# Performance work log

Measured on AMD Instinct MI355X. Metric: run time of the kernel, lower is better.

## Reference

```python
import jax, jax.numpy as jnp
import numpy as np

INPUT_LAYER_SIZE = 40960 * 2
LAYER1_SIZE = 512
LAYER2_SIZE = 32
LAYER3_SIZE = 32
BATCH = 4096


def setup_inputs() -> dict:
    key = jax.random.key(0)
    ks = jax.random.split(key, 10)
    # Sparse one-hot style features: mostly zeros with ~30 active entries per side.
    def sparse_features(k, n_active=30):
        kidx, = jax.random.split(k, 1)
        idx = jax.random.randint(kidx, (BATCH, n_active), 0, 40960)
        feats = jnp.zeros((BATCH, 40960), dtype=jnp.float32)
        return feats.at[jnp.arange(BATCH)[:, None], idx].set(1.0)
    w_features = sparse_features(ks[0])
    b_features = sparse_features(ks[1])
    s_in = 1.0 / np.sqrt(INPUT_LAYER_SIZE)
    s1 = 1.0 / np.sqrt(LAYER1_SIZE)
    s2 = 1.0 / np.sqrt(LAYER2_SIZE)
    s3 = 1.0 / np.sqrt(LAYER3_SIZE)
    return {
        "w_features": w_features,
        "b_features": b_features,
        "W_in": jax.random.uniform(ks[2], (LAYER1_SIZE, INPUT_LAYER_SIZE), jnp.float32, -s_in, s_in),
        "b_in": jax.random.uniform(ks[3], (LAYER1_SIZE,), jnp.float32, -s_in, s_in),
        "W1": jax.random.uniform(ks[4], (LAYER2_SIZE, LAYER1_SIZE), jnp.float32, -s1, s1),
        "b1": jax.random.uniform(ks[5], (LAYER2_SIZE,), jnp.float32, -s1, s1),
        "W2": jax.random.uniform(ks[6], (LAYER3_SIZE, LAYER2_SIZE), jnp.float32, -s2, s2),
        "b2": jax.random.uniform(ks[7], (LAYER3_SIZE,), jnp.float32, -s2, s2),
        "W3": jax.random.uniform(ks[8], (1, LAYER3_SIZE), jnp.float32, -s3, s3),
        "b3": jax.random.uniform(ks[9], (1,), jnp.float32, -s3, s3),
    }


def reference(w_features, b_features, W_in, b_in, W1, b1, W2, b2, W3, b3):
    # Concatenate both perspectives: [B, 81920]
    x = jnp.concatenate([w_features, b_features], axis=1)
    # Huge sparse-input accumulator layer (the kernel-headroom op)
    accum = x @ W_in.T + b_in                       # [B, 512]
    l1 = jnp.clip(accum, 0.0, 1.0)                  # clipped ReLU
    l2 = jnp.clip(l1 @ W1.T + b1, 0.0, 1.0)         # [B, 32]
    l3 = jnp.clip(l2 @ W2.T + b2, 0.0, 1.0)         # [B, 32]
    return l3 @ W3.T + b3                           # [B, 1]
```

## Files before the change

kernel.cpp:

```cpp
#include <hip/hip_runtime.h>
#include <hip/hip_bf16.h>

#define IN_PER_SIDE   40960
#define IN_TOTAL      81920
#define L1            512
#define L2            32
#define L3_           32
#define BATCH         4096
#define MAXIDX        128

typedef float    v4f __attribute__((ext_vector_type(4)));
typedef float    v8f __attribute__((ext_vector_type(8)));
typedef _Float16 v4h __attribute__((ext_vector_type(4)));
typedef _Float16 v8h __attribute__((ext_vector_type(8)));

#define WT_BYTES ((size_t)IN_TOTAL * L1 * sizeof(_Float16))

__global__ __launch_bounds__(256) void transpose_win(
    const float* __restrict__ W, _Float16* __restrict__ WTh)
{
    __shared__ float tile[64][65];
    const int jt = blockIdx.x * 64;
    const int ot = blockIdx.y * 64;
    const int tx = threadIdx.x & 15;
    const int ty = threadIdx.x >> 4;

#pragma unroll
    for (int k = 0; k < 4; ++k) {
        const int o = ty + 16 * k;
        const v4f* p = (const v4f*)&W[(size_t)(ot + o) * IN_TOTAL + jt + 4 * tx];
        v4f v = __builtin_nontemporal_load(p);
        tile[4 * tx + 0][o] = v.x;
        tile[4 * tx + 1][o] = v.y;
        tile[4 * tx + 2][o] = v.z;
        tile[4 * tx + 3][o] = v.w;
    }
    __syncthreads();
#pragma unroll
    for (int k = 0; k < 4; ++k) {
        const int j = ty + 16 * k;
        v4f v;
        v.x = tile[j][4 * tx + 0];
        v.y = tile[j][4 * tx + 1];
        v.z = tile[j][4 * tx + 2];
        v.w = tile[j][4 * tx + 3];
        v4h h = __builtin_convertvector(v, v4h);
        *(v4h*)&WTh[(size_t)(jt + j) * L1 + ot + 4 * tx] = h;
    }
}

__global__ __launch_bounds__(512) void nnue_fused(
    const float* __restrict__ wf, const float* __restrict__ bfeat,
    const _Float16* __restrict__ WTh,
    const float* __restrict__ b_in,
    const float* __restrict__ W1, const float* __restrict__ b1,
    const float* __restrict__ W2, const float* __restrict__ b2,
    const float* __restrict__ W3, const float* __restrict__ b3,
    float* __restrict__ out)
{
    const int b = blockIdx.x;
    const int t = threadIdx.x;

    __shared__ int   sidx[MAXIDX];
    __shared__ int   scnt;
    __shared__ float accs[8 * 64 * 9];
    __shared__ float l1s[L1];
    __shared__ float l2acc[L2];
    __shared__ float l2s[L2];
    __shared__ float l3s[L3_];

    if (t == 0) scnt = 0;
    __syncthreads();

    const v4f* wrow = (const v4f*)(wf    + (size_t)b * IN_PER_SIDE);
    const v4f* brow = (const v4f*)(bfeat + (size_t)b * IN_PER_SIDE);
    const int nvec = IN_PER_SIDE / 4;

    for (int i = t; i < nvec; i += 512) {
        v4f v = __builtin_nontemporal_load(wrow + i);
        if (v.x + v.y + v.z + v.w != 0.0f) {
            if (v.x != 0.0f) sidx[atomicAdd(&scnt, 1)] = 4 * i + 0;
            if (v.y != 0.0f) sidx[atomicAdd(&scnt, 1)] = 4 * i + 1;
            if (v.z != 0.0f) sidx[atomicAdd(&scnt, 1)] = 4 * i + 2;
            if (v.w != 0.0f) sidx[atomicAdd(&scnt, 1)] = 4 * i + 3;
        }
        v4f u = __builtin_nontemporal_load(brow + i);
        if (u.x + u.y + u.z + u.w != 0.0f) {
            if (u.x != 0.0f) sidx[atomicAdd(&scnt, 1)] = IN_PER_SIDE + 4 * i + 0;
            if (u.y != 0.0f) sidx[atomicAdd(&scnt, 1)] = IN_PER_SIDE + 4 * i + 1;
            if (u.z != 0.0f) sidx[atomicAdd(&scnt, 1)] = IN_PER_SIDE + 4 * i + 2;
            if (u.w != 0.0f) sidx[atomicAdd(&scnt, 1)] = IN_PER_SIDE + 4 * i + 3;
        }
    }
    __syncthreads();

    const int n = scnt;
    const int w = t >> 6;
    const int l = t & 63;
    const v8h* WTH8 = (const v8h*)WTh;

    v8f acc0 = {0,0,0,0,0,0,0,0};
    v8f acc1 = {0,0,0,0,0,0,0,0};
    int k = w;
    for (; k + 16 <= n; k += 16) {
        v8h h0 = WTH8[(size_t)sidx[k]     * 64 + l];
        v8h h1 = WTH8[(size_t)sidx[k + 8] * 64 + l];
        acc0 += __builtin_convertvector(h0, v8f);
        acc1 += __builtin_convertvector(h1, v8f);
    }
    for (; k < n; k += 8)
        acc0 += __builtin_convertvector(WTH8[(size_t)sidx[k] * 64 + l], v8f);
    acc0 += acc1;

    {
        float* dst = &accs[(w * 64 + l) * 9];
#pragma unroll
        for (int i = 0; i < 8; ++i) dst[i] = acc0[i];
    }
    __syncthreads();

    {
        const int ll = t >> 3, c = t & 7;
        float s = 0.0f;
#pragma unroll
        for (int ww = 0; ww < 8; ++ww) s += accs[(ww * 64 + ll) * 9 + c];
        l1s[t] = fminf(fmaxf(s + b_in[t], 0.0f), 1.0f);
    }
    __syncthreads();

    {
        const int kk = t >> 4;
        const int gg = t & 15;
        const float* wp = W1 + (size_t)kk * L1;
        float p = 0.0f;
        for (int o = gg; o < L1; o += 16) p += wp[o] * l1s[o];
#pragma unroll
        for (int off = 8; off > 0; off >>= 1) p += __shfl_down(p, off, 16);
        if (gg == 0) l2acc[kk] = p;
    }
    __syncthreads();
    if (t < L2) l2s[t] = fminf(fmaxf(l2acc[t] + b1[t], 0.0f), 1.0f);
    __syncthreads();

    if (t < L3_) {
        const float* wp = W2 + (size_t)t * L2;
        float p = b2[t];
#pragma unroll
        for (int q = 0; q < L2; ++q) p += wp[q] * l2s[q];
        l3s[t] = fminf(fmaxf(p, 0.0f), 1.0f);
    }
    __syncthreads();

    if (t == 0) {
        float p = b3[0];
#pragma unroll
        for (int q = 0; q < L3_; ++q) p += W3[q] * l3s[q];
        out[b] = p;
    }
}

__global__ __launch_bounds__(512) void nnue_fallback(
    const float* __restrict__ wf, const float* __restrict__ bfeat,
    const float* __restrict__ W_in, const float* __restrict__ b_in,
    const float* __restrict__ W1, const float* __restrict__ b1,
    const float* __restrict__ W2, const float* __restrict__ b2,
    const float* __restrict__ W3, const float* __restrict__ b3,
    float* __restrict__ out)
{
    const int b = blockIdx.x;
    const int t = threadIdx.x;
    __shared__ int   idxs[MAXIDX];
    __shared__ int   scnt;
    __shared__ float l1s[L1];
    __shared__ float l2acc[L2];
    __shared__ float l2s[L2];
    __shared__ float l3s[L3_];

    if (t == 0) scnt = 0;
    __syncthreads();
    const v4f* wrow = (const v4f*)(wf    + (size_t)b * IN_PER_SIDE);
    const v4f* brow = (const v4f*)(bfeat + (size_t)b * IN_PER_SIDE);
    for (int i = t; i < IN_PER_SIDE / 4; i += 512) {
        v4f v = wrow[i];
        if (v.x != 0.0f) idxs[atomicAdd(&scnt, 1)] = 4 * i + 0;
        if (v.y != 0.0f) idxs[atomicAdd(&scnt, 1)] = 4 * i + 1;
        if (v.z != 0.0f) idxs[atomicAdd(&scnt, 1)] = 4 * i + 2;
        if (v.w != 0.0f) idxs[atomicAdd(&scnt, 1)] = 4 * i + 3;
        v4f u = brow[i];
        if (u.x != 0.0f) idxs[atomicAdd(&scnt, 1)] = IN_PER_SIDE + 4 * i + 0;
        if (u.y != 0.0f) idxs[atomicAdd(&scnt, 1)] = IN_PER_SIDE + 4 * i + 1;
        if (u.z != 0.0f) idxs[atomicAdd(&scnt, 1)] = IN_PER_SIDE + 4 * i + 2;
        if (u.w != 0.0f) idxs[atomicAdd(&scnt, 1)] = IN_PER_SIDE + 4 * i + 3;
    }
    __syncthreads();
    const int n = scnt;
    float a0 = 0.0f;
    const float* row = W_in + (size_t)t * IN_TOTAL;
    for (int i = 0; i < n; ++i) a0 += row[idxs[i]];
    l1s[t] = fminf(fmaxf(b_in[t] + a0, 0.0f), 1.0f);
    __syncthreads();
    {
        const int k = t >> 4, g = t & 15;
        const float* wp = W1 + (size_t)k * L1;
        float p = 0.0f;
        for (int o = g; o < L1; o += 16) p += wp[o] * l1s[o];
#pragma unroll
        for (int off = 8; off > 0; off >>= 1) p += __shfl_down(p, off, 16);
        if (g == 0) l2acc[k] = p;
    }
    __syncthreads();
    if (t < L2) l2s[t] = fminf(fmaxf(l2acc[t] + b1[t], 0.0f), 1.0f);
    __syncthreads();
    if (t < L3_) {
        const float* wp = W2 + (size_t)t * L2;
        float p = b2[t];
#pragma unroll
        for (int q = 0; q < L2; ++q) p += wp[q] * l2s[q];
        l3s[t] = fminf(fmaxf(p, 0.0f), 1.0f);
    }
    __syncthreads();
    if (t == 0) {
        float p = b3[0];
#pragma unroll
        for (int q = 0; q < L3_; ++q) p += W3[q] * l3s[q];
        out[b] = p;
    }
}

extern "C" void kernel_launch(void* const* d_in, const int* in_sizes, int n_in,
                              void* d_out, int out_size, void* d_ws, size_t ws_size,
                              hipStream_t stream) {
    const float* wf   = (const float*)d_in[0];
    const float* bfeat= (const float*)d_in[1];
    const float* W_in = (const float*)d_in[2];
    const float* b_in = (const float*)d_in[3];
    const float* W1   = (const float*)d_in[4];
    const float* b1   = (const float*)d_in[5];
    const float* W2   = (const float*)d_in[6];
    const float* b2   = (const float*)d_in[7];
    const float* W3   = (const float*)d_in[8];
    const float* b3   = (const float*)d_in[9];
    float* out = (float*)d_out;

    if (ws_size >= WT_BYTES) {
        _Float16* WTh = (_Float16*)d_ws;
        dim3 grid(IN_TOTAL / 64, L1 / 64);
        transpose_win<<<grid, 256, 0, stream>>>(W_in, WTh);
        nnue_fused<<<BATCH, 512, 0, stream>>>(
            wf, bfeat, WTh, b_in, W1, b1, W2, b2, W3, b3, out);
    } else {
        nnue_fallback<<<BATCH, 512, 0, stream>>>(
            wf, bfeat, W_in, b_in, W1, b1, W2, b2, W3, b3, out);
    }
}
```

Before: 1.303 ms.

## Fuse weight transpose into main kernel with work-stealing tiles and global barrier

Merges the separate W_in transpose/fp16 conversion kernel into the main NNUE kernel: blocks dynamically claim transpose tiles through a global atomic counter, then scan their feature rows, then spin-wait until all tiles are done before gathering. The goal is to overlap the feature-row scanning with the transpose and remove a kernel launch boundary. It adds a memset launch, a grid-wide spin barrier that relies on all claiming blocks being resident or finishing (deadlock risk if the grid is oversubscribed and late blocks wait while unfinished tiles have not been claimed), and shared-memory union reuse.

```diff
diff --git a/kernel.cpp b/kernel.cpp
--- a/kernel.cpp
+++ b/kernel.cpp
@@ -8,6 +8,7 @@
 #define L3_           32
 #define BATCH         4096
 #define MAXIDX        128
+#define NTILES        10240
 
 typedef float    v4f __attribute__((ext_vector_type(4)));
 typedef float    v8f __attribute__((ext_vector_type(8)));
@@ -15,43 +16,12 @@
 typedef _Float16 v8h __attribute__((ext_vector_type(8)));
 
 #define WT_BYTES ((size_t)IN_TOTAL * L1 * sizeof(_Float16))
-
-__global__ __launch_bounds__(256) void transpose_win(
-    const float* __restrict__ W, _Float16* __restrict__ WTh)
-{
-    __shared__ float tile[64][65];
-    const int jt = blockIdx.x * 64;
-    const int ot = blockIdx.y * 64;
-    const int tx = threadIdx.x & 15;
-    const int ty = threadIdx.x >> 4;
-
-#pragma unroll
-    for (int k = 0; k < 4; ++k) {
-        const int o = ty + 16 * k;
-        const v4f* p = (const v4f*)&W[(size_t)(ot + o) * IN_TOTAL + jt + 4 * tx];
-        v4f v = __builtin_nontemporal_load(p);
-        tile[4 * tx + 0][o] = v.x;
-        tile[4 * tx + 1][o] = v.y;
-        tile[4 * tx + 2][o] = v.z;
-        tile[4 * tx + 3][o] = v.w;
-    }
-    __syncthreads();
-#pragma unroll
-    for (int k = 0; k < 4; ++k) {
-        const int j = ty + 16 * k;
-        v4f v;
-        v.x = tile[j][4 * tx + 0];
-        v.y = tile[j][4 * tx + 1];
-        v.z = tile[j][4 * tx + 2];
-        v.w = tile[j][4 * tx + 3];
-        v4h h = __builtin_convertvector(v, v4h);
-        *(v4h*)&WTh[(size_t)(jt + j) * L1 + ot + 4 * tx] = h;
-    }
-}
-
-__global__ __launch_bounds__(512) void nnue_fused(
+#define CTR_BYTES 128
+
+__global__ __launch_bounds__(512) void nnue_all(
+    const float* __restrict__ W, _Float16* __restrict__ WTh,
+    int* __restrict__ ctrs,
     const float* __restrict__ wf, const float* __restrict__ bfeat,
-    const _Float16* __restrict__ WTh,
     const float* __restrict__ b_in,
     const float* __restrict__ W1, const float* __restrict__ b1,
     const float* __restrict__ W2, const float* __restrict__ b2,
@@ -61,16 +31,60 @@
     const int b = blockIdx.x;
     const int t = threadIdx.x;
 
+    __shared__ union {
+        float tile[64][65];
+        float accs[8 * 64 * 9];
+    } sh;
     __shared__ int   sidx[MAXIDX];
     __shared__ int   scnt;
-    __shared__ float accs[8 * 64 * 9];
+    __shared__ int   stile;
     __shared__ float l1s[L1];
     __shared__ float l2acc[L2];
     __shared__ float l2s[L2];
     __shared__ float l3s[L3_];
 
+    int* claim_ctr = ctrs;
+    int* done_ctr  = ctrs + 16;
+
     if (t == 0) scnt = 0;
-    __syncthreads();
+
+    int my = 0;
+    for (;;) {
+        if (t == 0) stile = atomicAdd(claim_ctr, 1);
+        __syncthreads();
+        const int tile_id = stile;
+        if (tile_id >= NTILES) break;
+        ++my;
+        const int jt = (tile_id % 1280) * 64;
+        const int ot = (tile_id / 1280) * 64;
+        {
+            const int tx = t & 15, o = t >> 4;
+#pragma unroll
+            for (int k = 0; k < 2; ++k) {
+                const int oo = o + 32 * k;
+                const v4f* p = (const v4f*)&W[(size_t)(ot + oo) * IN_TOTAL + jt + 4 * tx];
+                v4f v = __builtin_nontemporal_load(p);
+                sh.tile[4 * tx + 0][oo] = v.x;
+                sh.tile[4 * tx + 1][oo] = v.y;
+                sh.tile[4 * tx + 2][oo] = v.z;
+                sh.tile[4 * tx + 3][oo] = v.w;
+            }
+        }
+        __syncthreads();
+        {
+            const int j = t >> 3, c0 = (t & 7) * 8;
+            v8f vf;
+#pragma unroll
+            for (int i = 0; i < 8; ++i) vf[i] = sh.tile[j][c0 + i];
+            v8h h = __builtin_convertvector(vf, v8h);
+            *(v8h*)&WTh[(size_t)(jt + j) * L1 + ot + c0] = h;
+        }
+        __syncthreads();
+    }
+    if (my > 0 && t == 0) {
+        __threadfence();
+        atomicAdd(done_ctr, my);
+    }
 
     const v4f* wrow = (const v4f*)(wf    + (size_t)b * IN_PER_SIDE);
     const v4f* brow = (const v4f*)(bfeat + (size_t)b * IN_PER_SIDE);
@@ -91,6 +105,13 @@
             if (u.z != 0.0f) sidx[atomicAdd(&scnt, 1)] = IN_PER_SIDE + 4 * i + 2;
             if (u.w != 0.0f) sidx[atomicAdd(&scnt, 1)] = IN_PER_SIDE + 4 * i + 3;
         }
+    }
+
+    if (t == 0) {
+        while (__hip_atomic_load(done_ctr, __ATOMIC_RELAXED,
+                                 __HIP_MEMORY_SCOPE_AGENT) < NTILES)
+            __builtin_amdgcn_s_sleep(2);
+        __threadfence();
     }
     __syncthreads();
 
@@ -113,7 +134,7 @@
     acc0 += acc1;
 
     {
-        float* dst = &accs[(w * 64 + l) * 9];
+        float* dst = &sh.accs[(w * 64 + l) * 9];
 #pragma unroll
         for (int i = 0; i < 8; ++i) dst[i] = acc0[i];
     }
@@ -123,7 +144,7 @@
         const int ll = t >> 3, c = t & 7;
         float s = 0.0f;
 #pragma unroll
-        for (int ww = 0; ww < 8; ++ww) s += accs[(ww * 64 + ll) * 9 + c];
+        for (int ww = 0; ww < 8; ++ww) s += sh.accs[(ww * 64 + ll) * 9 + c];
         l1s[t] = fminf(fmaxf(s + b_in[t], 0.0f), 1.0f);
     }
     __syncthreads();
@@ -242,12 +263,12 @@
     const float* b3   = (const float*)d_in[9];
     float* out = (float*)d_out;
 
-    if (ws_size >= WT_BYTES) {
+    if (ws_size >= WT_BYTES + CTR_BYTES) {
         _Float16* WTh = (_Float16*)d_ws;
-        dim3 grid(IN_TOTAL / 64, L1 / 64);
-        transpose_win<<<grid, 256, 0, stream>>>(W_in, WTh);
-        nnue_fused<<<BATCH, 512, 0, stream>>>(
-            wf, bfeat, WTh, b_in, W1, b1, W2, b2, W3, b3, out);
+        int* ctrs = (int*)((char*)d_ws + WT_BYTES);
+        hipMemsetAsync(ctrs, 0, CTR_BYTES, stream);
+        nnue_all<<<BATCH, 512, 0, stream>>>(
+            W_in, WTh, ctrs, wf, bfeat, b_in, W1, b1, W2, b2, W3, b3, out);
     } else {
         nnue_fallback<<<BATCH, 512, 0, stream>>>(
             wf, bfeat, W_in, b_in, W1, b1, W2, b2, W3, b3, out);
```

Result: slower. 1.625 ms (+24.7%).
